# Performance work log

Hardware: AMD Instinct MI355X
Metric: run time of the kernel (lower is better)

## Reference

```python
import jax, jax.numpy as jnp
import numpy as np
from jax import lax

B, S, MAX_WORD = 64, 40, 25
L = S * MAX_WORD            # 1000 tokens
D_IN, D = 768, 256
G = 6                       # lda_group_num
KW, KS = 5, 3               # word / sentence conv kernel sizes


def _conv1d(x, W, b, pad):
    # x: (B, Cin, L), W: (Cout, Cin, K) -> (B, Cout, L) ('same' via explicit pad)
    y = lax.conv_general_dilated(x, W, window_strides=(1,), padding=[(pad, pad)],
                                 dimension_numbers=('NCH', 'OIH', 'NCH'))
    return y + b[None, :, None]


def _mha(x, Wq, bq, Wk, bk, Wv, bv, Wo, bo):
    # single-head self-attention; x: (batch, seq, D)
    q = x @ Wq + bq
    k = x @ Wk + bk
    v = x @ Wv + bv
    scores = jnp.einsum('bqd,bkd->bqk', q, k) / jnp.sqrt(jnp.asarray(D, x.dtype))
    attn = jax.nn.softmax(scores, axis=-1)
    out = jnp.einsum('bqk,bkd->bqd', attn, v)
    return out @ Wo + bo


def setup_inputs() -> dict:
    key = jax.random.key(0)
    ks = jax.random.split(key, 32)
    s = 0.05
    p = lambda k, shape: jax.random.normal(k, shape, jnp.float32) * s
    x = jax.random.normal(ks[0], (B, D_IN, L), jnp.float32)
    lda = jax.random.randint(ks[1], (B, S), 0, G)
    # guarantee each group non-empty per row (original would NaN on empty groups)
    lda = lda.at[:, :G].set(jnp.broadcast_to(jnp.arange(G), (B, G)))
    inp = {'x': x, 'lda_groups': lda,
           'Wc_w': p(ks[2], (D, D_IN, KW)), 'bc_w': p(ks[3], (D,)),
           'Wq_w': p(ks[4], (D, D)), 'bq_w': p(ks[5], (D,)),
           'Wk_w': p(ks[6], (D, D)), 'bk_w': p(ks[7], (D,)),
           'Wv_w': p(ks[8], (D, D)), 'bv_w': p(ks[9], (D,)),
           'Wo_w': p(ks[10], (D, D)), 'bo_w': p(ks[11], (D,)),
           'Wc_s': p(ks[12], (D, D, KS)), 'bc_s': p(ks[13], (D,)),
           'Wq_s': p(ks[14], (D, D)), 'bq_s': p(ks[15], (D,)),
           'Wk_s': p(ks[16], (D, D)), 'bk_s': p(ks[17], (D,)),
           'Wv_s': p(ks[18], (D, D)), 'bv_s': p(ks[19], (D,)),
           'Wo_s': p(ks[20], (D, D)), 'bo_s': p(ks[21], (D,)),
           'Wq_a': p(ks[22], (D, D)), 'bq_a': p(ks[23], (D,)),
           'Wk_a': p(ks[24], (D, D)), 'bk_a': p(ks[25], (D,)),
           'Wv_a': p(ks[26], (D, D)), 'bv_a': p(ks[27], (D,)),
           'Wo_a': p(ks[28], (D, D)), 'bo_a': p(ks[29], (D,))}
    return inp


def reference(x, lda_groups, Wc_w, bc_w, Wq_w, bq_w, Wk_w, bk_w, Wv_w, bv_w, Wo_w, bo_w,
              Wc_s, bc_s, Wq_s, bq_s, Wk_s, bk_s, Wv_s, bv_s, Wo_s, bo_s,
              Wq_a, bq_a, Wk_a, bk_a, Wv_a, bv_a, Wo_a, bo_a):
    # word-level CNN (dropout = identity in eval) + attention gate
    h = jax.nn.relu(_conv1d(x, Wc_w, bc_w, (KW - 1) // 2))      # (B, D, L)
    h = jnp.transpose(h, (0, 2, 1))                              # (B, L, D)
    h = h * _mha(h, Wq_w, bq_w, Wk_w, bk_w, Wv_w, bv_w, Wo_w, bo_w)
    # word_level_mean: contiguous blocks of MAX_WORD words -> sentence vectors
    h = h.reshape(B, S, MAX_WORD, D).mean(axis=2)                # (B, S, D)
    # sentence-level CNN
    h = jnp.transpose(h, (0, 2, 1))
    h = jax.nn.relu(_conv1d(h, Wc_s, bc_s, (KS - 1) // 2))
    h = jnp.transpose(h, (0, 2, 1))                              # (B, S, D)
    # sentence attention: torch MHA has batch_first=False but gets (B,S,D),
    # i.e. it attends over the batch axis with S as batch -> transpose
    ht = jnp.transpose(h, (1, 0, 2))
    a = jnp.transpose(_mha(ht, Wq_s, bq_s, Wk_s, bk_s, Wv_s, bv_s, Wo_s, bo_s), (1, 0, 2))
    h = h * a
    # aspect_level_mean (faithful to the original bug): per (batch, group) the
    # mean is a SCALAR over selected sentences AND all channels, broadcast to D
    mask = (lda_groups[:, :, None] == jnp.arange(G)[None, None, :]).astype(h.dtype)  # (B,S,G)
    gsum = jnp.einsum('bs,bsg->bg', h.sum(-1), mask)
    cnt = mask.sum(axis=1) * D
    ha = jnp.broadcast_to((gsum / cnt)[:, :, None], (B, G, D))   # (B, G, D)
    # aspect attention applied twice with the SAME params; same batch_first quirk
    for _ in range(2):
        hat = jnp.transpose(ha, (1, 0, 2))
        a = jnp.transpose(_mha(hat, Wq_a, bq_a, Wk_a, bk_a, Wv_a, bv_a, Wo_a, bo_a), (1, 0, 2))
        ha = ha * a
    return ha
```

## Files before the change

### kernel.cpp

```cpp
#include <hip/hip_runtime.h>
#include <hip/hip_bf16.h>


typedef unsigned short u16;
typedef __attribute__((ext_vector_type(8))) short bf16x8;
typedef __attribute__((ext_vector_type(4))) float f32x4;
typedef __attribute__((ext_vector_type(4))) unsigned short u16x4;
typedef __attribute__((ext_vector_type(8))) unsigned short u16x8;

__device__ __forceinline__ float bf2f(u16 u) {
  union { float f; unsigned int i; } x; x.i = ((unsigned int)u) << 16; return x.f;
}
__device__ __forceinline__ u16 f2bf(float f) {
  union { float f; unsigned int i; } x; x.f = f;
  unsigned int i = x.i;
  i += 0x7FFFu + ((i >> 16) & 1u);
  return (u16)(i >> 16);
}
__device__ __forceinline__ void gload16(const u16* g, u16* l) {
  __builtin_amdgcn_global_load_lds(
      (const __attribute__((address_space(1))) unsigned int*)g,
      (__attribute__((address_space(3))) unsigned int*)l, 16, 0, 0);
}

__global__ __launch_bounds__(256) void prep_weights_kernel(
    const float* __restrict__ Wc_w, const float* __restrict__ Wq_w,
    const float* __restrict__ Wk_w, const float* __restrict__ Wv_w,
    const float* __restrict__ Wo_w, const float* __restrict__ bq_w,
    const float* __restrict__ bk_w, const float* __restrict__ bv_w,
    const float* __restrict__ Wc_s,
    u16* __restrict__ WtT, u16* __restrict__ WqkvT, u16* __restrict__ WoT,
    float* __restrict__ bqkv, float* __restrict__ Wts)
{
  int idx = blockIdx.x * 256 + threadIdx.x;
  if (idx < 983040) {
    int n = idx / 3840, kk = idx % 3840;
    int k = kk / 768, c = kk % 768;
    WtT[idx] = f2bf(Wc_w[n * 3840 + c * 5 + k]);
  }
  if (idx < 196608) {
    int n = idx >> 8, kd = idx & 255;
    float v = (n < 256) ? Wq_w[kd * 256 + n]
            : (n < 512) ? Wk_w[kd * 256 + (n - 256)]
                        : Wv_w[kd * 256 + (n - 512)];
    WqkvT[idx] = f2bf(v);
  }
  if (idx < 65536) {
    int n = idx >> 8, kd = idx & 255;
    WoT[idx] = f2bf(Wo_w[kd * 256 + n]);
  }
  if (idx < 768) {
    bqkv[idx] = (idx < 256) ? bq_w[idx] : (idx < 512) ? bk_w[idx - 256] : bv_w[idx - 512];
  }
  if (idx < 196608) {
    int kk = idx >> 8, d = idx & 255;
    int k = kk >> 8, dc = kk & 255;
    Wts[idx] = Wc_s[d * 768 + dc * 3 + k];
  }
}

__global__ __launch_bounds__(256) void zero_pad_kernel(u16* __restrict__ xT)
{
  int c8 = blockIdx.x * 256 + threadIdx.x;
  if (c8 >= 172032) return;
  int e = c8 * 8;
  int b = e / 21504, rem = e % 21504;
  int rowi = rem / 768, c = rem % 768;
  int row = (rowi < 2) ? rowi : (1000 + rowi);
  u16x8 z = {0, 0, 0, 0, 0, 0, 0, 0};
  *(u16x8*)&xT[((size_t)b * 1028 + row) * 768 + c] = z;
}

__global__ __launch_bounds__(256) void transpose_x_kernel(const float* __restrict__ x,
                                                          u16* __restrict__ xT)
{
  __shared__ float lds[64][65];
  int t = threadIdx.x;
  int bid = blockIdx.x;
  int b = bid / 192, rem = bid % 192;
  int c0 = (rem / 16) * 64, l0 = (rem % 16) * 64;
  int pr = t >> 4, plc = (t & 15) * 4;
  #pragma unroll
  for (int i = 0; i < 4; i++) {
    int r = i * 16 + pr;
    f32x4 v = {0.f, 0.f, 0.f, 0.f};
    if (l0 + plc < 1000)
      v = *(const f32x4*)&x[((size_t)b * 768 + c0 + r) * 1000 + l0 + plc];
    lds[r][plc + 0] = v[0]; lds[r][plc + 1] = v[1];
    lds[r][plc + 2] = v[2]; lds[r][plc + 3] = v[3];
  }
  __syncthreads();
  int qr = t >> 3, qc = (t & 7) * 8;
  #pragma unroll
  for (int i = 0; i < 2; i++) {
    int l = i * 32 + qr;
    if (l0 + l < 1000) {
      u16x8 o;
      #pragma unroll
      for (int j = 0; j < 8; j++) o[j] = f2bf(lds[qc + j][l]);
      *(u16x8*)&xT[((size_t)b * 1028 + 2 + l0 + l) * 768 + c0 + qc] = o;
    }
  }
}

__global__ __launch_bounds__(256) void transpose_v_kernel(const u16* __restrict__ qkv,
                                                          u16* __restrict__ vT)
{
  __shared__ u16 lds[64][65];
  int t = threadIdx.x;
  int b = blockIdx.x >> 6, rem = blockIdx.x & 63;
  int d0 = (rem >> 4) * 64, kv0 = (rem & 15) * 64;
  int pr = t >> 4, plc = (t & 15) * 4;
  #pragma unroll
  for (int i = 0; i < 4; i++) {
    int kvl = i * 16 + pr;
    int kv = kv0 + kvl;
    u16x4 v = {0, 0, 0, 0};
    if (kv < 1000)
      v = *(const u16x4*)&qkv[((size_t)(b * 1000) + kv) * 768 + 512 + d0 + plc];
    lds[kvl][plc + 0] = v[0]; lds[kvl][plc + 1] = v[1];
    lds[kvl][plc + 2] = v[2]; lds[kvl][plc + 3] = v[3];
  }
  __syncthreads();
  int qr = t >> 3, qc = (t & 7) * 8;
  #pragma unroll
  for (int i = 0; i < 2; i++) {
    int d = i * 32 + qr;
    u16x8 o;
    #pragma unroll
    for (int j = 0; j < 8; j++) o[j] = lds[qc + j][d];
    *(u16x8*)&vT[((size_t)(b * 256) + d0 + d) * 1024 + kv0 + qc] = o;
  }
}

template<bool CONV, bool RELU>
__global__ __launch_bounds__(256, 2) void gemm_bf16_kernel(
    const u16* __restrict__ A, const u16* __restrict__ Bt,
    const float* __restrict__ bias, u16* __restrict__ C,
    int lda, int K, int nk, int ntiles, int ldc)
{
  __shared__ u16 Alds[2][64 * 64];
  __shared__ u16 Blds[2][256 * 64];
  int t = threadIdx.x;
  int wave = t >> 6, lane = t & 63;
  int l15 = lane & 15, l4 = lane >> 4;
  int mt = blockIdx.x / ntiles, nt = blockIdx.x % ntiles;
  int wn = wave * 64;

  unsigned int aoff[2]; int aldsoff[2];
  #pragma unroll
  for (int i = 0; i < 2; i++) {
    int c = wave * 2 + i;
    int lr = c * 8 + (lane >> 3);
    int ss = (lane & 7) ^ (lr & 7);
    int gm = mt * 64 + lr;
    unsigned int base;
    if (CONV) base = (unsigned int)((gm >> 10) * 789504 + (gm & 1023) * 768);
    else      base = (unsigned int)gm * (unsigned int)lda;
    aoff[i] = base + (unsigned int)(ss * 8);
    aldsoff[i] = c * 512;
  }
  unsigned int boff[8]; int bldsoff[8];
  #pragma unroll
  for (int i = 0; i < 8; i++) {
    int c = wave * 8 + i;
    int lr = c * 8 + (lane >> 3);
    int ss = (lane & 7) ^ (lr & 7);
    boff[i] = (unsigned int)(nt * 256 + lr) * (unsigned int)K + (unsigned int)(ss * 8);
    bldsoff[i] = c * 512;
  }

  f32x4 acc[4][4];
  #pragma unroll
  for (int mf = 0; mf < 4; mf++)
    #pragma unroll
    for (int nf = 0; nf < 4; nf++) acc[mf][nf] = f32x4{0.f, 0.f, 0.f, 0.f};

  #pragma unroll
  for (int i = 0; i < 2; i++) gload16(A + aoff[i], &Alds[0][aldsoff[i]]);
  #pragma unroll
  for (int i = 0; i < 8; i++) gload16(Bt + boff[i], &Blds[0][bldsoff[i]]);
  __syncthreads();

  int cur = 0;
  for (int ks = 0; ks < nk; ks++) {
    if (ks + 1 < nk) {
      unsigned int ko = (unsigned int)(ks + 1) * 64u;
      #pragma unroll
      for (int i = 0; i < 2; i++) gload16(A + aoff[i] + ko, &Alds[cur ^ 1][aldsoff[i]]);
      #pragma unroll
      for (int i = 0; i < 8; i++) gload16(Bt + boff[i] + ko, &Blds[cur ^ 1][bldsoff[i]]);
    }
    const u16* Ab = &Alds[cur][0];
    const u16* Bb = &Blds[cur][0];
    #pragma unroll
    for (int kc = 0; kc < 2; kc++) {
      int q = kc * 4 + l4;
      bf16x8 af[4], bfr[4];
      #pragma unroll
      for (int mf = 0; mf < 4; mf++) {
        int r = mf * 16 + l15;
        af[mf] = *(const bf16x8*)(&Ab[r * 64 + ((q ^ (r & 7)) * 8)]);
      }
      #pragma unroll
      for (int nf = 0; nf < 4; nf++) {
        int rb = wn + nf * 16 + l15;
        bfr[nf] = *(const bf16x8*)(&Bb[rb * 64 + ((q ^ (rb & 7)) * 8)]);
      }
      #pragma unroll
      for (int mf = 0; mf < 4; mf++)
        #pragma unroll
        for (int nf = 0; nf < 4; nf++)
          acc[mf][nf] = __builtin_amdgcn_mfma_f32_16x16x32_bf16(af[mf], bfr[nf], acc[mf][nf], 0, 0, 0);
    }
    __syncthreads();
    cur ^= 1;
  }
  float bv[4];
  #pragma unroll
  for (int nf = 0; nf < 4; nf++) bv[nf] = bias[nt * 256 + wn + nf * 16 + l15];
  #pragma unroll
  for (int mf = 0; mf < 4; mf++) {
    #pragma unroll
    for (int r = 0; r < 4; r++) {
      int rowl = mf * 16 + l4 * 4 + r;
      int gm = mt * 64 + rowl;
      size_t orow; bool ok = true;
      if (CONV) { int bb = gm >> 10, ll = gm & 1023; ok = (ll < 1000); orow = (size_t)bb * 1000 + ll; }
      else orow = (size_t)gm;
      if (ok) {
        #pragma unroll
        for (int nf = 0; nf < 4; nf++) {
          float v = acc[mf][nf][r] + bv[nf];
          if (RELU) v = fmaxf(v, 0.f);
          C[orow * ldc + nt * 256 + wn + nf * 16 + l15] = f2bf(v);
        }
      }
    }
  }
}

__global__ __launch_bounds__(256, 3) void flash_kernel(
    const u16* __restrict__ qkv, const u16* __restrict__ vT, u16* __restrict__ ctx)
{
  __shared__ u16 Klds[32 * 256];
  __shared__ u16 Vlds[256 * 32];
  __shared__ u16 Plds[4 * 640];
  int t = threadIdx.x, wave = t >> 6, lane = t & 63;
  int l15 = lane & 15, l4 = lane >> 4;
  int b = blockIdx.x >> 4, qt = blockIdx.x & 15;

  int qrow = qt * 64 + wave * 16 + l15;
  const u16* qp = qkv + ((size_t)(b * 1000) + qrow) * 768;
  bf16x8 qreg[8];
  #pragma unroll
  for (int kk = 0; kk < 8; kk++) qreg[kk] = *(const bf16x8*)(qp + kk * 32 + l4 * 8);

  f32x4 acc[16];
  #pragma unroll
  for (int df = 0; df < 16; df++) acc[df] = f32x4{0.f, 0.f, 0.f, 0.f};
  float tsum[4] = {0.f, 0.f, 0.f, 0.f};

  const u16* ksrc[4]; int kdst[4];
  const u16* vsrc[4]; int vdst[4];
  #pragma unroll
  for (int i = 0; i < 4; i++) {
    int c = i * 256 + t;
    int kr = c >> 5, kslot = c & 31;
    ksrc[i] = qkv + ((size_t)(b * 1000 + kr)) * 768 + 256 + kslot * 8;
    kdst[i] = kr * 256 + ((kslot ^ (kr & 7)) * 8);
    int vd = c >> 2, vslot = c & 3;
    vsrc[i] = vT + ((size_t)(b * 256 + vd)) * 1024 + vslot * 8;
    vdst[i] = vd * 32 + ((vslot ^ (vd & 3)) * 8);
  }
  bf16x8 kreg[4], vreg[4];
  #pragma unroll
  for (int i = 0; i < 4; i++) { kreg[i] = *(const bf16x8*)ksrc[i]; vreg[i] = *(const bf16x8*)vsrc[i]; }

  u16* pl = &Plds[wave * 640];

  for (int tile = 0; tile < 32; tile++) {
    __syncthreads();
    #pragma unroll
    for (int i = 0; i < 4; i++) {
      *(bf16x8*)(&Klds[kdst[i]]) = kreg[i];
      *(bf16x8*)(&Vlds[vdst[i]]) = vreg[i];
    }
    __syncthreads();
    if (tile + 1 < 32) {
      #pragma unroll
      for (int i = 0; i < 4; i++) {
        kreg[i] = *(const bf16x8*)(ksrc[i] + (size_t)(tile + 1) * 32 * 768);
        vreg[i] = *(const bf16x8*)(vsrc[i] + (tile + 1) * 32);
      }
    }
    f32x4 s[2];
    #pragma unroll
    for (int cf = 0; cf < 2; cf++) {
      s[cf] = f32x4{0.f, 0.f, 0.f, 0.f};
      int kr = cf * 16 + l15;
      #pragma unroll
      for (int kk = 0; kk < 8; kk++) {
        bf16x8 kf = *(const bf16x8*)(&Klds[kr * 256 + (((kk * 4 + l4) ^ (kr & 7)) * 8)]);
        s[cf] = __builtin_amdgcn_mfma_f32_16x16x32_bf16(qreg[kk], kf, s[cf], 0, 0, 0);
      }
    }
    int colb = tile * 32;
    float pv[2][4];
    #pragma unroll
    for (int r = 0; r < 4; r++) {
      float s0 = s[0][r] * 0.0625f;
      float s1 = s[1][r] * 0.0625f;
      if (colb + l15 >= 1000)      s0 = -1e30f;
      if (colb + 16 + l15 >= 1000) s1 = -1e30f;
      float p0 = __expf(s0 - 20.f);
      float p1 = __expf(s1 - 20.f);
      tsum[r] += p0 + p1;
      pv[0][r] = p0; pv[1][r] = p1;
    }
    #pragma unroll
    for (int cf = 0; cf < 2; cf++)
      #pragma unroll
      for (int r = 0; r < 4; r++)
        pl[(l4 * 4 + r) * 40 + cf * 16 + l15] = f2bf(pv[cf][r]);
    bf16x8 pa = *(const bf16x8*)(&pl[l15 * 40 + l4 * 8]);
    #pragma unroll
    for (int df = 0; df < 16; df++) {
      int d = df * 16 + l15;
      bf16x8 vf = *(const bf16x8*)(&Vlds[d * 32 + ((l4 ^ (d & 3)) * 8)]);
      acc[df] = __builtin_amdgcn_mfma_f32_16x16x32_bf16(pa, vf, acc[df], 0, 0, 0);
    }
  }
  #pragma unroll
  for (int r = 0; r < 4; r++) {
    float ts = tsum[r];
    #pragma unroll
    for (int mk = 1; mk < 16; mk <<= 1) ts += __shfl_xor(ts, mk, 16);
    tsum[r] = ts;
  }
  int orow0 = qt * 64 + wave * 16 + l4 * 4;
  #pragma unroll
  for (int r = 0; r < 4; r++) {
    int orow = orow0 + r;
    if (orow < 1000) {
      float inv = 1.0f / tsum[r];
      size_t base = ((size_t)(b * 1000) + orow) * 256;
      #pragma unroll
      for (int df = 0; df < 16; df++)
        ctx[base + df * 16 + l15] = f2bf(acc[df][r] * inv);
    }
  }
}

__global__ __launch_bounds__(256) void gate_mean_kernel(const u16* __restrict__ h,
                                                        const u16* __restrict__ ao,
                                                        u16* __restrict__ hmpad)
{
  int r = blockIdx.x, t = threadIdx.x;
  int b = r / 40, s = r % 40;
  size_t base = ((size_t)b * 1000 + s * 25) * 256 + t;
  float acc = 0.f;
  #pragma unroll 5
  for (int w = 0; w < 25; w++) acc += bf2f(h[base + (size_t)w * 256]) * bf2f(ao[base + (size_t)w * 256]);
  hmpad[((size_t)b * 42 + 1 + s) * 256 + t] = f2bf(acc * 0.04f);
}

__global__ __launch_bounds__(256) void sent_conv_kernel(const u16* __restrict__ hmpad,
                                                        const float* __restrict__ Wts,
                                                        const float* __restrict__ bc_s,
                                                        float* __restrict__ hs)
{
  __shared__ float alds[10 * 256];
  int t = threadIdx.x;
  int b = blockIdx.x / 5, s0 = (blockIdx.x % 5) * 8;
  #pragma unroll
  for (int i = 0; i < 10; i++)
    alds[i * 256 + t] = bf2f(hmpad[((size_t)b * 42 + s0 + i) * 256 + t]);
  __syncthreads();
  float acc[8]; float bv = bc_s[t];
  #pragma unroll
  for (int j = 0; j < 8; j++) acc[j] = bv;
  for (int kk = 0; kk < 768; kk++) {
    float w = Wts[(size_t)kk * 256 + t];
    #pragma unroll
    for (int j = 0; j < 8; j++) acc[j] += alds[j * 256 + kk] * w;
  }
  #pragma unroll
  for (int j = 0; j < 8; j++)
    hs[((size_t)b * 40 + s0 + j) * 256 + t] = fmaxf(acc[j], 0.f);
}

__global__ __launch_bounds__(256) void proj3_kernel(
    const float* __restrict__ A,
    const float* __restrict__ Wq, const float* __restrict__ bq,
    const float* __restrict__ Wk, const float* __restrict__ bk,
    const float* __restrict__ Wv, const float* __restrict__ bv,
    float* __restrict__ oq, float* __restrict__ okk, float* __restrict__ ov,
    int nb, int GS)
{
  __shared__ float alds[8 * 256];
  int sel = blockIdx.x / nb;
  int m0 = (blockIdx.x % nb) * 8;
  const float* W = (sel == 0) ? Wq : (sel == 1) ? Wk : Wv;
  const float* bias_ = (sel == 0) ? bq : (sel == 1) ? bk : bv;
  float* out = (sel == 0) ? oq : (sel == 1) ? okk : ov;
  int t = threadIdx.x;
  #pragma unroll
  for (int i = 0; i < 8; i++) {
    int r = m0 + i;
    int src = (r & 63) * GS + (r >> 6);
    alds[i * 256 + t] = A[(size_t)src * 256 + t];
  }
  __syncthreads();
  float acc[8]; float bv_ = bias_[t];
  #pragma unroll
  for (int i = 0; i < 8; i++) acc[i] = bv_;
  for (int k = 0; k < 256; k++) {
    float w = W[(size_t)k * 256 + t];
    #pragma unroll
    for (int i = 0; i < 8; i++) acc[i] += alds[i * 256 + k] * w;
  }
  #pragma unroll
  for (int i = 0; i < 8; i++) out[((size_t)m0 + i) * 256 + t] = acc[i];
}

__global__ __launch_bounds__(256) void attn_fused_kernel(
    const float* __restrict__ q, const float* __restrict__ k,
    const float* __restrict__ v, const float* __restrict__ Wo,
    const float* __restrict__ bo, const float* __restrict__ gate_src,
    float* __restrict__ out, int GS)
{
  __shared__ float pbuf[4][64];
  __shared__ float pvals[64];
  __shared__ float obuf[256];
  int r = blockIdx.x;
  int bb = r >> 6, i = r & 63;
  int t = threadIdx.x, tj = t & 63, part = t >> 6;
  const float* qrow = q + (size_t)r * 256 + part * 64;
  const float* krow = k + ((size_t)(bb * 64) + tj) * 256 + part * 64;
  float pp = 0.f;
  #pragma unroll 16
  for (int kk = 0; kk < 64; kk++) pp += qrow[kk] * krow[kk];
  pbuf[part][tj] = pp;
  __syncthreads();
  if (t < 64) {
    float s = (pbuf[0][t] + pbuf[1][t] + pbuf[2][t] + pbuf[3][t]) * 0.0625f;
    float mx = s;
    #pragma unroll
    for (int mk = 1; mk < 64; mk <<= 1) mx = fmaxf(mx, __shfl_xor(mx, mk, 64));
    float p = __expf(s - mx);
    float sm = p;
    #pragma unroll
    for (int mk = 1; mk < 64; mk <<= 1) sm += __shfl_xor(sm, mk, 64);
    pvals[t] = p / sm;
  }
  __syncthreads();
  float acc = 0.f;
  const float* vb = v + (size_t)(bb * 64) * 256 + t;
  for (int j = 0; j < 64; j++) acc += pvals[j] * vb[(size_t)j * 256];
  obuf[t] = acc;
  __syncthreads();
  float o = bo[t];
  for (int kk = 0; kk < 256; kk++) o += obuf[kk] * Wo[(size_t)kk * 256 + t];
  size_t gi = (size_t)i * GS + bb;
  out[gi * 256 + t] = gate_src[gi * 256 + t] * o;
}

__global__ __launch_bounds__(256) void aspect_mean_kernel(const float* __restrict__ h2,
                                                          const int* __restrict__ ldaG,
                                                          float* __restrict__ ha0)
{
  __shared__ float partbuf[6][256];
  __shared__ int ldas[40];
  __shared__ float gval[6];
  int b = blockIdx.x, t = threadIdx.x;
  if (t < 40) ldas[t] = ldaG[b * 40 + t];
  __syncthreads();
  float part[6] = {0, 0, 0, 0, 0, 0};
  for (int idx = t; idx < 10240; idx += 256) {
    int s = idx >> 8, d = idx & 255;
    float v = h2[((size_t)b * 40 + s) * 256 + d];
    int g = ldas[s];
    #pragma unroll
    for (int gg = 0; gg < 6; gg++) if (g == gg) part[gg] += v;
  }
  #pragma unroll
  for (int g = 0; g < 6; g++) partbuf[g][t] = part[g];
  __syncthreads();
  if (t < 6) {
    float ssum = 0.f;
    for (int i = 0; i < 256; i++) ssum += partbuf[t][i];
    int cnt = 0;
    for (int s = 0; s < 40; s++) cnt += (ldas[s] == t) ? 1 : 0;
    gval[t] = ssum / ((float)cnt * 256.0f);
  }
  __syncthreads();
  #pragma unroll
  for (int g = 0; g < 6; g++) ha0[((size_t)b * 6 + g) * 256 + t] = gval[g];
}

extern "C" void kernel_launch(void* const* d_in, const int* in_sizes, int n_in,
                              void* d_out, int out_size, void* d_ws, size_t ws_size,
                              hipStream_t stream) {
  (void)in_sizes; (void)n_in; (void)out_size; (void)ws_size;
  const float* x    = (const float*)d_in[0];
  const int*   ldaG = (const int*)d_in[1];
  const float* Wc_w = (const float*)d_in[2];
  const float* bc_w = (const float*)d_in[3];
  const float* Wq_w = (const float*)d_in[4];
  const float* bq_w = (const float*)d_in[5];
  const float* Wk_w = (const float*)d_in[6];
  const float* bk_w = (const float*)d_in[7];
  const float* Wv_w = (const float*)d_in[8];
  const float* bv_w = (const float*)d_in[9];
  const float* Wo_w = (const float*)d_in[10];
  const float* bo_w = (const float*)d_in[11];
  const float* Wc_s = (const float*)d_in[12];
  const float* bc_s = (const float*)d_in[13];
  const float* Wq_s = (const float*)d_in[14];
  const float* bq_s = (const float*)d_in[15];
  const float* Wk_s = (const float*)d_in[16];
  const float* bk_s = (const float*)d_in[17];
  const float* Wv_s = (const float*)d_in[18];
  const float* bv_s = (const float*)d_in[19];
  const float* Wo_s = (const float*)d_in[20];
  const float* bo_s = (const float*)d_in[21];
  const float* Wq_a = (const float*)d_in[22];
  const float* bq_a = (const float*)d_in[23];
  const float* Wk_a = (const float*)d_in[24];
  const float* bk_a = (const float*)d_in[25];
  const float* Wv_a = (const float*)d_in[26];
  const float* bv_a = (const float*)d_in[27];
  const float* Wo_a = (const float*)d_in[28];
  const float* bo_a = (const float*)d_in[29];

  char* ws = (char*)d_ws;
  u16*  xT    = (u16*)(ws + 0);
  u16*  qkvb  = (u16*)(ws + 0);
  u16*  attno = (u16*)(ws + 0);
  u16*  WtT   = (u16*)(ws + 101056512ULL);
  u16*  WqkvT = (u16*)(ws + 103022592ULL);
  u16*  WoT   = (u16*)(ws + 103415808ULL);
  float* bqkv = (float*)(ws + 103546880ULL);
  float* Wts  = (float*)(ws + 103549952ULL);
  u16*  h     = (u16*)(ws + 104336384ULL);
  u16*  ctx   = (u16*)(ws + 137104384ULL);
  u16*  vT    = (u16*)(ws + 169872384ULL);
  u16*  hmpad = (u16*)(ws + 203426816ULL);
  float* hs   = (float*)(ws + 204803072ULL);
  float* sq   = (float*)(ws + 207424512ULL);
  float* sk   = (float*)(ws + 210045952ULL);
  float* sv   = (float*)(ws + 212667392ULL);
  float* h2   = (float*)(ws + 215288832ULL);
  float* ha0  = (float*)(ws + 217910272ULL);
  float* aq   = (float*)(ws + 218303488ULL);
  float* ak   = (float*)(ws + 218696704ULL);
  float* av   = (float*)(ws + 219089920ULL);
  float* ha1  = (float*)(ws + 219483136ULL);

  hipMemsetAsync(hmpad, 0, 1376256ULL, stream);
  zero_pad_kernel<<<672, 256, 0, stream>>>(xT);

  prep_weights_kernel<<<3840, 256, 0, stream>>>(Wc_w, Wq_w, Wk_w, Wv_w, Wo_w,
                                                bq_w, bk_w, bv_w, Wc_s,
                                                WtT, WqkvT, WoT, bqkv, Wts);
  transpose_x_kernel<<<12288, 256, 0, stream>>>(x, xT);
  gemm_bf16_kernel<true, true><<<1024, 256, 0, stream>>>(xT, WtT, bc_w, h, 768, 3840, 60, 1, 256);
  gemm_bf16_kernel<false, false><<<3000, 256, 0, stream>>>(h, WqkvT, bqkv, qkvb, 256, 256, 4, 3, 768);
  transpose_v_kernel<<<4096, 256, 0, stream>>>(qkvb, vT);
  flash_kernel<<<1024, 256, 0, stream>>>(qkvb, vT, ctx);
  gemm_bf16_kernel<false, false><<<1000, 256, 0, stream>>>(ctx, WoT, bo_w, attno, 256, 256, 4, 1, 256);
  gate_mean_kernel<<<2560, 256, 0, stream>>>(h, attno, hmpad);
  sent_conv_kernel<<<320, 256, 0, stream>>>(hmpad, Wts, bc_s, hs);
  proj3_kernel<<<960, 256, 0, stream>>>(hs, Wq_s, bq_s, Wk_s, bk_s, Wv_s, bv_s,
                                        sq, sk, sv, 320, 40);
  attn_fused_kernel<<<2560, 256, 0, stream>>>(sq, sk, sv, Wo_s, bo_s, hs, h2, 40);
  aspect_mean_kernel<<<64, 256, 0, stream>>>(h2, ldaG, ha0);

  const float* hacur = ha0;
  for (int it = 0; it < 2; it++) {
    proj3_kernel<<<144, 256, 0, stream>>>(hacur, Wq_a, bq_a, Wk_a, bk_a, Wv_a, bv_a,
                                          aq, ak, av, 48, 6);
    float* dst = (it == 0) ? ha1 : (float*)d_out;
    attn_fused_kernel<<<384, 256, 0, stream>>>(aq, ak, av, Wo_a, bo_a, hacur, dst, 6);
    hacur = dst;
  }
}
```

Baseline: 705.2 us.

## Switch GEMM to 32x32 MFMA, single-buffer B tile, raise occupancy

```diff
diff --git a/kernel.cpp b/kernel.cpp
--- a/kernel.cpp
+++ b/kernel.cpp
@@ -5,6 +5,7 @@
 typedef unsigned short u16;
 typedef __attribute__((ext_vector_type(8))) short bf16x8;
 typedef __attribute__((ext_vector_type(4))) float f32x4;
+typedef __attribute__((ext_vector_type(16))) float f32x16;
 typedef __attribute__((ext_vector_type(4))) unsigned short u16x4;
 typedef __attribute__((ext_vector_type(8))) unsigned short u16x8;
 
@@ -134,16 +135,16 @@
 }
 
 template<bool CONV, bool RELU>
-__global__ __launch_bounds__(256, 2) void gemm_bf16_kernel(
+__global__ __launch_bounds__(256, 3) void gemm_bf16_kernel(
     const u16* __restrict__ A, const u16* __restrict__ Bt,
     const float* __restrict__ bias, u16* __restrict__ C,
     int lda, int K, int nk, int ntiles, int ldc)
 {
   __shared__ u16 Alds[2][64 * 64];
-  __shared__ u16 Blds[2][256 * 64];
+  __shared__ u16 Blds[256 * 64];
   int t = threadIdx.x;
   int wave = t >> 6, lane = t & 63;
-  int l15 = lane & 15, l4 = lane >> 4;
+  int l31 = lane & 31, lhi = lane >> 5;
   int mt = blockIdx.x / ntiles, nt = blockIdx.x % ntiles;
   int wn = wave * 64;
 
@@ -170,70 +171,71 @@
     bldsoff[i] = c * 512;
   }
 
-  f32x4 acc[4][4];
-  #pragma unroll
-  for (int mf = 0; mf < 4; mf++)
-    #pragma unroll
-    for (int nf = 0; nf < 4; nf++) acc[mf][nf] = f32x4{0.f, 0.f, 0.f, 0.f};
+  f32x16 acc[2][2];
+  #pragma unroll
+  for (int mi = 0; mi < 2; mi++)
+    #pragma unroll
+    for (int ni = 0; ni < 2; ni++)
+      #pragma unroll
+      for (int e = 0; e < 16; e++) acc[mi][ni][e] = 0.f;
 
   #pragma unroll
   for (int i = 0; i < 2; i++) gload16(A + aoff[i], &Alds[0][aldsoff[i]]);
-  #pragma unroll
-  for (int i = 0; i < 8; i++) gload16(Bt + boff[i], &Blds[0][bldsoff[i]]);
-  __syncthreads();
 
   int cur = 0;
   for (int ks = 0; ks < nk; ks++) {
+    unsigned int ko = (unsigned int)ks * 64u;
+    #pragma unroll
+    for (int i = 0; i < 8; i++) gload16(Bt + boff[i] + ko, &Blds[bldsoff[i]]);
     if (ks + 1 < nk) {
-      unsigned int ko = (unsigned int)(ks + 1) * 64u;
-      #pragma unroll
-      for (int i = 0; i < 2; i++) gload16(A + aoff[i] + ko, &Alds[cur ^ 1][aldsoff[i]]);
-      #pragma unroll
-      for (int i = 0; i < 8; i++) gload16(Bt + boff[i] + ko, &Blds[cur ^ 1][bldsoff[i]]);
-    }
+      #pragma unroll
+      for (int i = 0; i < 2; i++) gload16(A + aoff[i] + ko + 64u, &Alds[cur ^ 1][aldsoff[i]]);
+      asm volatile("s_waitcnt vmcnt(2)" ::: "memory");
+    } else {
+      asm volatile("s_waitcnt vmcnt(0)" ::: "memory");
+    }
+    __builtin_amdgcn_s_barrier();
     const u16* Ab = &Alds[cur][0];
-    const u16* Bb = &Blds[cur][0];
-    #pragma unroll
-    for (int kc = 0; kc < 2; kc++) {
-      int q = kc * 4 + l4;
-      bf16x8 af[4], bfr[4];
-      #pragma unroll
-      for (int mf = 0; mf < 4; mf++) {
-        int r = mf * 16 + l15;
-        af[mf] = *(const bf16x8*)(&Ab[r * 64 + ((q ^ (r & 7)) * 8)]);
+    #pragma unroll
+    for (int kst = 0; kst < 4; kst++) {
+      int q = kst * 2 + lhi;
+      bf16x8 af[2], bfr[2];
+      #pragma unroll
+      for (int mi = 0; mi < 2; mi++) {
+        int r = mi * 32 + l31;
+        af[mi] = *(const bf16x8*)(&Ab[r * 64 + ((q ^ (r & 7)) * 8)]);
       }
       #pragma unroll
-      for (int nf = 0; nf < 4; nf++) {
-        int rb = wn + nf * 16 + l15;
-        bfr[nf] = *(const bf16x8*)(&Bb[rb * 64 + ((q ^ (rb & 7)) * 8)]);
+      for (int ni = 0; ni < 2; ni++) {
+        int rb = wn + ni * 32 + l31;
+        bfr[ni] = *(const bf16x8*)(&Blds[rb * 64 + ((q ^ (rb & 7)) * 8)]);
       }
       #pragma unroll
-      for (int mf = 0; mf < 4; mf++)
+      for (int mi = 0; mi < 2; mi++)
         #pragma unroll
-        for (int nf = 0; nf < 4; nf++)
-          acc[mf][nf] = __builtin_amdgcn_mfma_f32_16x16x32_bf16(af[mf], bfr[nf], acc[mf][nf], 0, 0, 0);
-    }
-    __syncthreads();
+        for (int ni = 0; ni < 2; ni++)
+          acc[mi][ni] = __builtin_amdgcn_mfma_f32_32x32x16_bf16(af[mi], bfr[ni], acc[mi][ni], 0, 0, 0);
+    }
+    __builtin_amdgcn_s_barrier();
     cur ^= 1;
   }
-  float bv[4];
-  #pragma unroll
-  for (int nf = 0; nf < 4; nf++) bv[nf] = bias[nt * 256 + wn + nf * 16 + l15];
-  #pragma unroll
-  for (int mf = 0; mf < 4; mf++) {
-    #pragma unroll
-    for (int r = 0; r < 4; r++) {
-      int rowl = mf * 16 + l4 * 4 + r;
-      int gm = mt * 64 + rowl;
-      size_t orow; bool ok = true;
-      if (CONV) { int bb = gm >> 10, ll = gm & 1023; ok = (ll < 1000); orow = (size_t)bb * 1000 + ll; }
-      else orow = (size_t)gm;
-      if (ok) {
-        #pragma unroll
-        for (int nf = 0; nf < 4; nf++) {
-          float v = acc[mf][nf][r] + bv[nf];
+
+  #pragma unroll
+  for (int mi = 0; mi < 2; mi++) {
+    #pragma unroll
+    for (int ni = 0; ni < 2; ni++) {
+      float bb = bias[nt * 256 + wn + ni * 32 + l31];
+      #pragma unroll
+      for (int reg = 0; reg < 16; reg++) {
+        int row_in = (reg & 3) + 8 * (reg >> 2) + 4 * lhi;
+        int gm = mt * 64 + mi * 32 + row_in;
+        size_t orow; bool ok = true;
+        if (CONV) { int bb2 = gm >> 10, ll = gm & 1023; ok = (ll < 1000); orow = (size_t)bb2 * 1000 + ll; }
+        else orow = (size_t)gm;
+        if (ok) {
+          float v = acc[mi][ni][reg] + bb;
           if (RELU) v = fmaxf(v, 0.f);
-          C[orow * ldc + nt * 256 + wn + nf * 16 + l15] = f2bf(v);
+          C[orow * ldc + nt * 256 + wn + ni * 32 + l31] = f2bf(v);
         }
       }
     }
```

New measurement: 723.1 us. +2.5%, slower.

## Replace im2col conv GEMM with tap-reuse kernel and single-buffer GEMMs

Applied to the files above, without the earlier changes.

```diff
diff --git a/kernel.cpp b/kernel.cpp
--- a/kernel.cpp
+++ b/kernel.cpp
@@ -133,14 +133,108 @@
   }
 }
 
-template<bool CONV, bool RELU>
-__global__ __launch_bounds__(256, 2) void gemm_bf16_kernel(
+__global__ __launch_bounds__(256, 3) void conv_tap_kernel(
+    const u16* __restrict__ A, const u16* __restrict__ Bt,
+    const float* __restrict__ bias, u16* __restrict__ C)
+{
+  __shared__ u16 strip[96 * 64];
+  __shared__ u16 Blds[256 * 64];
+  int t = threadIdx.x;
+  int wave = t >> 6, lane = t & 63;
+  int l15 = lane & 15, l4 = lane >> 4;
+  int mt = blockIdx.x;
+  int wn = wave * 64;
+
+  unsigned int aoff[3]; int aldsoff[3];
+  #pragma unroll
+  for (int i = 0; i < 3; i++) {
+    int rc = wave * 3 + i;
+    int lr = rc * 8 + (lane >> 3);
+    int ss = (lane & 7) ^ (lr & 7);
+    int gm = mt * 64 + lr;
+    aoff[i] = (unsigned int)((gm >> 10) * 789504 + (gm & 1023) * 768 + ss * 8);
+    aldsoff[i] = rc * 512;
+  }
+  unsigned int boff[8]; int bldsoff[8];
+  #pragma unroll
+  for (int i = 0; i < 8; i++) {
+    int c = wave * 8 + i;
+    int lr = c * 8 + (lane >> 3);
+    int ss = (lane & 7) ^ (lr & 7);
+    boff[i] = (unsigned int)(lr * 3840 + ss * 8);
+    bldsoff[i] = c * 512;
+  }
+
+  f32x4 acc[4][4];
+  #pragma unroll
+  for (int mf = 0; mf < 4; mf++)
+    #pragma unroll
+    for (int nf = 0; nf < 4; nf++) acc[mf][nf] = f32x4{0.f, 0.f, 0.f, 0.f};
+
+  for (int ch = 0; ch < 12; ch++) {
+    unsigned int co = (unsigned int)(ch * 64);
+    #pragma unroll
+    for (int i = 0; i < 3; i++) gload16(A + aoff[i] + co, &strip[aldsoff[i]]);
+    #pragma unroll 1
+    for (int tap = 0; tap < 5; tap++) {
+      unsigned int bo = (unsigned int)(tap * 768) + co;
+      #pragma unroll
+      for (int i = 0; i < 8; i++) gload16(Bt + boff[i] + bo, &Blds[bldsoff[i]]);
+      __syncthreads();
+      #pragma unroll
+      for (int kc = 0; kc < 2; kc++) {
+        int q = kc * 4 + l4;
+        bf16x8 af[4], bfr[4];
+        #pragma unroll
+        for (int mf = 0; mf < 4; mf++) {
+          int rr = mf * 16 + l15 + tap;
+          af[mf] = *(const bf16x8*)(&strip[rr * 64 + ((q ^ (rr & 7)) * 8)]);
+        }
+        #pragma unroll
+        for (int nf = 0; nf < 4; nf++) {
+          int rb = wn + nf * 16 + l15;
+          bfr[nf] = *(const bf16x8*)(&Blds[rb * 64 + ((q ^ (rb & 7)) * 8)]);
+        }
+        #pragma unroll
+        for (int mf = 0; mf < 4; mf++)
+          #pragma unroll
+          for (int nf = 0; nf < 4; nf++)
+            acc[mf][nf] = __builtin_amdgcn_mfma_f32_16x16x32_bf16(af[mf], bfr[nf], acc[mf][nf], 0, 0, 0);
+      }
+      __syncthreads();
+    }
+  }
+
+  float bv[4];
+  #pragma unroll
+  for (int nf = 0; nf < 4; nf++) bv[nf] = bias[wn + nf * 16 + l15];
+  #pragma unroll
+  for (int mf = 0; mf < 4; mf++) {
+    #pragma unroll
+    for (int r = 0; r < 4; r++) {
+      int rowl = mf * 16 + l4 * 4 + r;
+      int gm = mt * 64 + rowl;
+      int bb = gm >> 10, ll = gm & 1023;
+      if (ll < 1000) {
+        size_t orow = (size_t)bb * 1000 + ll;
+        #pragma unroll
+        for (int nf = 0; nf < 4; nf++) {
+          float v = fmaxf(acc[mf][nf][r] + bv[nf], 0.f);
+          C[orow * 256 + wn + nf * 16 + l15] = f2bf(v);
+        }
+      }
+    }
+  }
+}
+
+template<bool RELU>
+__global__ __launch_bounds__(256, 3) void gemm_bf16_kernel(
     const u16* __restrict__ A, const u16* __restrict__ Bt,
     const float* __restrict__ bias, u16* __restrict__ C,
     int lda, int K, int nk, int ntiles, int ldc)
 {
-  __shared__ u16 Alds[2][64 * 64];
-  __shared__ u16 Blds[2][256 * 64];
+  __shared__ u16 Alds[64 * 64];
+  __shared__ u16 Blds[256 * 64];
   int t = threadIdx.x;
   int wave = t >> 6, lane = t & 63;
   int l15 = lane & 15, l4 = lane >> 4;
@@ -154,10 +248,7 @@
     int lr = c * 8 + (lane >> 3);
     int ss = (lane & 7) ^ (lr & 7);
     int gm = mt * 64 + lr;
-    unsigned int base;
-    if (CONV) base = (unsigned int)((gm >> 10) * 789504 + (gm & 1023) * 768);
-    else      base = (unsigned int)gm * (unsigned int)lda;
-    aoff[i] = base + (unsigned int)(ss * 8);
+    aoff[i] = (unsigned int)gm * (unsigned int)lda + (unsigned int)(ss * 8);
     aldsoff[i] = c * 512;
   }
   unsigned int boff[8]; int bldsoff[8];
@@ -176,23 +267,13 @@
     #pragma unroll
     for (int nf = 0; nf < 4; nf++) acc[mf][nf] = f32x4{0.f, 0.f, 0.f, 0.f};
 
-  #pragma unroll
-  for (int i = 0; i < 2; i++) gload16(A + aoff[i], &Alds[0][aldsoff[i]]);
-  #pragma unroll
-  for (int i = 0; i < 8; i++) gload16(Bt + boff[i], &Blds[0][bldsoff[i]]);
-  __syncthreads();
-
-  int cur = 0;
   for (int ks = 0; ks < nk; ks++) {
-    if (ks + 1 < nk) {
-      unsigned int ko = (unsigned int)(ks + 1) * 64u;
-      #pragma unroll
-      for (int i = 0; i < 2; i++) gload16(A + aoff[i] + ko, &Alds[cur ^ 1][aldsoff[i]]);
-      #pragma unroll
-      for (int i = 0; i < 8; i++) gload16(Bt + boff[i] + ko, &Blds[cur ^ 1][bldsoff[i]]);
-    }
-    const u16* Ab = &Alds[cur][0];
-    const u16* Bb = &Blds[cur][0];
+    unsigned int ko = (unsigned int)ks * 64u;
+    #pragma unroll
+    for (int i = 0; i < 2; i++) gload16(A + aoff[i] + ko, &Alds[aldsoff[i]]);
+    #pragma unroll
+    for (int i = 0; i < 8; i++) gload16(Bt + boff[i] + ko, &Blds[bldsoff[i]]);
+    __syncthreads();
     #pragma unroll
     for (int kc = 0; kc < 2; kc++) {
       int q = kc * 4 + l4;
@@ -200,12 +281,12 @@
       #pragma unroll
       for (int mf = 0; mf < 4; mf++) {
         int r = mf * 16 + l15;
-        af[mf] = *(const bf16x8*)(&Ab[r * 64 + ((q ^ (r & 7)) * 8)]);
+        af[mf] = *(const bf16x8*)(&Alds[r * 64 + ((q ^ (r & 7)) * 8)]);
       }
       #pragma unroll
       for (int nf = 0; nf < 4; nf++) {
         int rb = wn + nf * 16 + l15;
-        bfr[nf] = *(const bf16x8*)(&Bb[rb * 64 + ((q ^ (rb & 7)) * 8)]);
+        bfr[nf] = *(const bf16x8*)(&Blds[rb * 64 + ((q ^ (rb & 7)) * 8)]);
       }
       #pragma unroll
       for (int mf = 0; mf < 4; mf++)
@@ -214,7 +295,6 @@
           acc[mf][nf] = __builtin_amdgcn_mfma_f32_16x16x32_bf16(af[mf], bfr[nf], acc[mf][nf], 0, 0, 0);
     }
     __syncthreads();
-    cur ^= 1;
   }
   float bv[4];
   #pragma unroll
@@ -224,23 +304,18 @@
     #pragma unroll
     for (int r = 0; r < 4; r++) {
       int rowl = mf * 16 + l4 * 4 + r;
-      int gm = mt * 64 + rowl;
-      size_t orow; bool ok = true;
-      if (CONV) { int bb = gm >> 10, ll = gm & 1023; ok = (ll < 1000); orow = (size_t)bb * 1000 + ll; }
-      else orow = (size_t)gm;
-      if (ok) {
-        #pragma unroll
-        for (int nf = 0; nf < 4; nf++) {
-          float v = acc[mf][nf][r] + bv[nf];
-          if (RELU) v = fmaxf(v, 0.f);
-          C[orow * ldc + nt * 256 + wn + nf * 16 + l15] = f2bf(v);
-        }
+      size_t orow = (size_t)(mt * 64 + rowl);
+      #pragma unroll
+      for (int nf = 0; nf < 4; nf++) {
+        float v = acc[mf][nf][r] + bv[nf];
+        if (RELU) v = fmaxf(v, 0.f);
+        C[orow * ldc + nt * 256 + wn + nf * 16 + l15] = f2bf(v);
       }
     }
   }
 }
 
-__global__ __launch_bounds__(256, 3) void flash_kernel(
+__global__ __launch_bounds__(256, 4) void flash_kernel(
     const u16* __restrict__ qkv, const u16* __restrict__ vT, u16* __restrict__ ctx)
 {
   __shared__ u16 Klds[32 * 256];
@@ -565,11 +640,11 @@
                                                 bq_w, bk_w, bv_w, Wc_s,
                                                 WtT, WqkvT, WoT, bqkv, Wts);
   transpose_x_kernel<<<12288, 256, 0, stream>>>(x, xT);
-  gemm_bf16_kernel<true, true><<<1024, 256, 0, stream>>>(xT, WtT, bc_w, h, 768, 3840, 60, 1, 256);
-  gemm_bf16_kernel<false, false><<<3000, 256, 0, stream>>>(h, WqkvT, bqkv, qkvb, 256, 256, 4, 3, 768);
+  conv_tap_kernel<<<1024, 256, 0, stream>>>(xT, WtT, bc_w, h);
+  gemm_bf16_kernel<false><<<3000, 256, 0, stream>>>(h, WqkvT, bqkv, qkvb, 256, 256, 4, 3, 768);
   transpose_v_kernel<<<4096, 256, 0, stream>>>(qkvb, vT);
   flash_kernel<<<1024, 256, 0, stream>>>(qkvb, vT, ctx);
-  gemm_bf16_kernel<false, false><<<1000, 256, 0, stream>>>(ctx, WoT, bo_w, attno, 256, 256, 4, 1, 256);
+  gemm_bf16_kernel<false><<<1000, 256, 0, stream>>>(ctx, WoT, bo_w, attno, 256, 256, 4, 1, 256);
   gate_mean_kernel<<<2560, 256, 0, stream>>>(h, attno, hmpad);
   sent_conv_kernel<<<320, 256, 0, stream>>>(hmpad, Wts, bc_s, hs);
   proj3_kernel<<<960, 256, 0, stream>>>(hs, Wq_s, bq_s, Wk_s, bk_s, Wv_s, bv_s,
```

Result: slower. 895.4 us (+27.0%).
